# Performance work log

Hardware: AMD Instinct MI355X
Metric: run time of the kernel (lower is better)

Reference implementation:

```python
import jax, jax.numpy as jnp
import numpy as np

B, TE, TD, EH, DH = 128, 512, 128, 512, 512
K_CNN, C_CNN = 7, 105

def setup_inputs() -> dict:
    key = jax.random.key(0)
    ks = jax.random.split(key, 20)
    n = lambda k, shp: jax.random.normal(k, shp, dtype=jnp.float32) * 0.05
    return {
        "LSTM": jax.random.normal(ks[0], (B, TE, EH), dtype=jnp.float32),
        "CNNs": jax.random.normal(ks[1], (B, K_CNN, C_CNN), dtype=jnp.float32),
        "Wa_w": n(ks[2], (TD, DH)), "Wa_b": n(ks[3], (TD,)),
        "Ua_w": n(ks[4], (TE, EH)), "Ua_b": n(ks[5], (TE,)),
        "va_w": n(ks[6], (1, TE + TD)), "va_b": n(ks[7], (1,)),
        "phi_w": n(ks[8], (EH, TE)), "phi_b": n(ks[9], (EH,)),
        "Wih": n(ks[10], (4 * DH, C_CNN + EH)), "Whh": n(ks[11], (4 * DH, DH)),
        "bih": n(ks[12], (4 * DH,)), "bhh": n(ks[13], (4 * DH,)),
        "wij_w": n(ks[14], (K_CNN, DH + C_CNN)), "wij_b": n(ks[15], (K_CNN,)),
        "s_i": jax.random.uniform(ks[16], (B, DH), dtype=jnp.float32),
        "m_i": jax.random.uniform(ks[17], (B, DH), dtype=jnp.float32),
    }

def reference(LSTM, CNNs, Wa_w, Wa_b, Ua_w, Ua_b, va_w, va_b, phi_w, phi_b,
              Wih, Whh, bih, bhh, wij_w, wij_b, s_i, m_i):
    Bn, Te, Eh = LSTM.shape
    Td = Wa_w.shape[0]
    Dh = s_i.shape[1]
    # delta_i_j for all j: strict lower-triangular one-hots [Te, Te]
    Dm = jnp.tril(jnp.ones((Te, Te), LSTM.dtype), k=-1)
    phi = Dm @ phi_w.T + phi_b                     # [Te, Eh]
    ph = phi[None, :, :] * LSTM                    # [B, Te, Eh] phi_delta * LSTM[:, j]
    Ua = jnp.einsum('bte,se->bts', ph, Ua_w) + Ua_b  # [B, Te, Te]
    Wa = s_i @ Wa_w.T + Wa_b                       # [B, Td] (same for all i, j)
    cat = jnp.concatenate([jnp.broadcast_to(Wa[:, None, :], (Bn, Te, Td)), Ua], axis=-1)
    Cw = jnp.tanh(cat) * va_w[0]                   # [B, Te, Td+Te]
    # one-hot mask picks index i + Te - j; v_a reduces to a single gathered term + bias
    idx = jnp.arange(Td)[:, None] + Te - jnp.arange(Te)[None, :]   # [Td, Te]
    e = Cw[:, jnp.arange(Te)[None, :], idx] + va_b[0]              # [B, Td, Te]
    a = jax.nn.softmax(e, axis=-1)
    c_i = jnp.einsum('bit,bte->bie', a, LSTM)      # [B, Td, Eh]
    # CNN attention (same for all decoder steps; note non-standard normalizer kept faithfully)
    w_cnn, w_s = wij_w[:, :C_CNN], wij_w[:, C_CNN:]
    ep = jnp.tanh(jnp.einsum('bkc,kc->bk', CNNs, w_cnn) + s_i @ w_s.T + wij_b)  # [B, K]
    ap = jnp.exp(ep) / jnp.sum(ep)
    c_p = jnp.einsum('bk,bkc->bc', ap, CNNs)       # [B, C_CNN]
    # LSTMCell with fixed (s_i, m_i) state => all decoder steps vectorize over i
    x = jnp.concatenate([c_i, jnp.broadcast_to(c_p[:, None, :], (Bn, Td, C_CNN))], axis=-1)
    gates = jnp.einsum('bid,gd->big', x, Wih) + bih + (s_i @ Whh.T + bhh)[:, None, :]
    ig, fg, gg, og = jnp.split(gates, 4, axis=-1)
    cnew = jax.nn.sigmoid(fg) * m_i[:, None, :] + jax.nn.sigmoid(ig) * jnp.tanh(gg)
    h = jax.nn.sigmoid(og) * jnp.tanh(cnew)        # [B, Td, Dh]
    return h
```

## Files before the change

kernel.cpp:

```cpp
#include <hip/hip_runtime.h>
#include <hip/hip_bf16.h>

#define B_   128
#define TE_  512
#define TD_  128
#define EH_  512
#define DH_  512
#define KC_  7
#define CC_  105
#define G_   2048
#define KX_  617
#define KP_  640
#define GNT  10

typedef __attribute__((ext_vector_type(8))) short bf16x8;
typedef __attribute__((ext_vector_type(4))) float f32x4;

__device__ __forceinline__ float sigm(float x){ return 1.f/(1.f + __expf(-x)); }
__device__ __forceinline__ float tanhf_fast(float x){
  float e = __expf(2.f*x);
  return 1.f - 2.f/(e + 1.f);
}

__device__ __forceinline__ unsigned short f2bf(float f){
  unsigned int u = __float_as_uint(f);
  unsigned int r = (u + 0x7fffu + ((u >> 16) & 1u)) >> 16;
  return (unsigned short)r;
}

typedef __attribute__((address_space(3))) unsigned int lds_u32_t;
typedef __attribute__((address_space(1))) const unsigned int glb_u32_t;
__device__ __forceinline__ void gload16(const void* g, void* l) {
  __builtin_amdgcn_global_load_lds((glb_u32_t*)g, (lds_u32_t*)l, 16, 0, 0);
}

static const size_t OFF_PHI  = 0;
static const size_t OFF_WA   = OFF_PHI  + (size_t)TE_*EH_*4;
static const size_t OFF_HPRE = OFF_WA   + (size_t)B_*TD_*4;
static const size_t OFF_EP   = OFF_HPRE + (size_t)B_*G_*4;
static const size_t OFF_CP   = OFF_EP   + 4096;
static const size_t OFF_ET   = ((OFF_CP + (size_t)B_*CC_*4 + 255)/256)*256;
static const size_t OFF_STAT = OFF_ET + (size_t)B_*TE_*TD_*4;
static const size_t OFF_P    = ((OFF_STAT + (size_t)2*B_*TD_*4 + 255)/256)*256;
static const size_t OFF_LT   = OFF_P  + (size_t)B_*TD_*TE_*2;
static const size_t OFF_WR   = OFF_LT + (size_t)B_*TE_*EH_*2;
static const size_t OFF_PT   = OFF_P;
static const size_t OFF_SUM  = OFF_PT + (size_t)TE_*EH_*4;
static const size_t OFF_WT   = OFF_P + (size_t)2*1024*1024;
static const size_t OFF_WAT  = OFF_P + (size_t)6*1024*1024;

__global__ __launch_bounds__(256) void k_tr(const float* __restrict__ src,
                                            float* __restrict__ dst, int R, int C) {
  int r0 = blockIdx.x * 64, c0 = blockIdx.y * 64;
  __shared__ float tile[64][65];
  int tid = threadIdx.x;
  int r = tid >> 2, c16 = (tid & 3) * 16;
  const float4* s4 = (const float4*)(src + (size_t)(r0 + r)*C + c0 + c16);
  float4 v0 = s4[0], v1 = s4[1], v2 = s4[2], v3 = s4[3];
  *(float4*)&tile[r][c16]    = v0;
  *(float4*)&tile[r][c16+4]  = v1;
  *(float4*)&tile[r][c16+8]  = v2;
  *(float4*)&tile[r][c16+12] = v3;
  __syncthreads();
  float o[16];
  #pragma unroll
  for (int j = 0; j < 16; ++j) o[j] = tile[c16+j][r];
  float* d = dst + (size_t)(c0 + r)*R + r0 + c16;
  *(float4*)d      = *(float4*)&o[0];
  *(float4*)(d+4)  = *(float4*)&o[4];
  *(float4*)(d+8)  = *(float4*)&o[8];
  *(float4*)(d+12) = *(float4*)&o[12];
}

__global__ void k_phiA(const float* __restrict__ phiT, float* __restrict__ phi,
                       float* __restrict__ sums) {
  int e = blockIdx.x * 256 + threadIdx.x;
  int z = blockIdx.y;
  float acc = 0.f;
  for (int t = z*64; t < z*64 + 64; ++t) {
    phi[(size_t)t*EH_ + e] = acc;
    acc += phiT[(size_t)t*EH_ + e];
  }
  sums[z*EH_ + e] = acc;
}
__global__ void k_phiB(const float* __restrict__ sums, const float* __restrict__ phi_b,
                       float* __restrict__ phi) {
  int e = blockIdx.x * 256 + threadIdx.x;
  int z = blockIdx.y;
  float off = phi_b[e];
  for (int zz = 0; zz < z; ++zz) off += sums[zz*EH_ + e];
  for (int t = z*64; t < z*64 + 64; ++t)
    phi[(size_t)t*EH_ + e] += off;
}

__global__ __launch_bounds__(256) void k_wa2(const float* __restrict__ s_i,
                                             const float* __restrict__ WaT,
                                             const float* __restrict__ Wa_b,
                                             const float* __restrict__ va_w,
                                             float* __restrict__ wa) {
  int lane = threadIdx.x & 63, wv = threadIdx.x >> 6;
  int b = blockIdx.x * 4 + wv;
  int d0 = lane * 2;
  const float2* w = (const float2*)WaT + lane;
  const float* s = s_i + (size_t)b*DH_;
  float ax = 0.f, ay = 0.f;
  #pragma unroll 8
  for (int k = 0; k < DH_; ++k) {
    float2 wv2 = w[(size_t)k*64];
    float x = s[k];
    ax += wv2.x * x; ay += wv2.y * x;
  }
  wa[b*TD_ + d0]     = tanhf_fast(ax + Wa_b[d0])     * va_w[d0];
  wa[b*TD_ + d0 + 1] = tanhf_fast(ay + Wa_b[d0 + 1]) * va_w[d0 + 1];
}

__global__ __launch_bounds__(256) void k_hpre2(const float* __restrict__ s_i,
                                               const float* __restrict__ WhhT,
                                               const float* __restrict__ bih,
                                               const float* __restrict__ bhh,
                                               float* __restrict__ hpre) {
  int gq = blockIdx.x * 256 + threadIdx.x;
  int b  = blockIdx.y;
  const float4* w = (const float4*)WhhT + gq;
  const float* s = s_i + (size_t)b*DH_;
  float4 a = {0.f,0.f,0.f,0.f};
  #pragma unroll 8
  for (int k = 0; k < DH_; ++k) {
    float4 wv = w[(size_t)k*512];
    float x = s[k];
    a.x += wv.x*x; a.y += wv.y*x; a.z += wv.z*x; a.w += wv.w*x;
  }
  int g = gq * 4;
  float4 bi = *(const float4*)(bih + g);
  float4 bh = *(const float4*)(bhh + g);
  float4 o;
  o.x = a.x + bi.x + bh.x; o.y = a.y + bi.y + bh.y;
  o.z = a.z + bi.z + bh.z; o.w = a.w + bi.w + bh.w;
  *(float4*)(hpre + (size_t)b*G_ + g) = o;
}

__global__ __launch_bounds__(256) void k_ep(const float* __restrict__ CNNs,
                                            const float* __restrict__ wij_w,
                                            const float* __restrict__ wij_b,
                                            const float* __restrict__ s_i,
                                            float* __restrict__ ep) {
  int gw = blockIdx.x * 4 + (threadIdx.x >> 6);
  int lane = threadIdx.x & 63;
  if (gw >= B_*KC_) return;
  int b = gw / KC_, k = gw % KC_;
  const float* cr = CNNs + (size_t)(b*KC_ + k)*CC_;
  const float* wr = wij_w + (size_t)k*KX_;
  float acc = 0.f;
  for (int c = lane; c < CC_; c += 64) acc += cr[c] * wr[c];
  const float* sr = s_i + (size_t)b*DH_;
  const float* wsr = wr + CC_;
  #pragma unroll
  for (int j = 0; j < 8; ++j) { int h = lane + j*64; acc += sr[h] * wsr[h]; }
  #pragma unroll
  for (int m = 32; m; m >>= 1) acc += __shfl_xor(acc, m, 64);
  if (lane == 0) ep[gw] = tanhf_fast(acc + wij_b[k]);
}

__global__ void k_epsum(const float* __restrict__ ep, float* __restrict__ epsum) {
  __shared__ float red[1024];
  int tid = threadIdx.x;
  red[tid] = (tid < B_*KC_) ? ep[tid] : 0.f;
  __syncthreads();
  for (int off = 512; off > 0; off >>= 1) {
    if (tid < off) red[tid] += red[tid + off];
    __syncthreads();
  }
  if (tid == 0) epsum[0] = red[0];
}

__global__ __launch_bounds__(128) void k_cp(const float* __restrict__ ep,
                                            const float* __restrict__ epsum,
                                            const float* __restrict__ CNNs,
                                            unsigned short* __restrict__ X) {
  int b = blockIdx.x, c = threadIdx.x;
  float S = epsum[0];
  float apl[KC_];
  #pragma unroll
  for (int k = 0; k < KC_; ++k) apl[k] = __expf(ep[b*KC_ + k]) / S;
  float acc = 0.f;
  if (c < CC_) {
    #pragma unroll
    for (int k = 0; k < KC_; ++k)
      acc += apl[k] * CNNs[(size_t)(b*KC_ + k)*CC_ + c];
  }
  unsigned short o = (c < CC_) ? f2bf(acc) : 0;
  unsigned short* xb = X + (size_t)b*TD_*KP_ + EH_ + c;
  for (int i = 0; i < TD_; ++i)
    xb[(size_t)i*KP_] = o;
}

__global__ void k_cvtW(const float* __restrict__ Wih, unsigned short* __restrict__ Wr) {
  int id = blockIdx.x * 256 + threadIdx.x;
  int nr = id / 80, c8 = (id % 80) * 8;
  int gate = nr & 3, dh = nr >> 2;
  const float* src = Wih + (size_t)(gate*DH_ + dh)*KX_;
  unsigned short o[8];
  #pragma unroll
  for (int j = 0; j < 8; ++j) {
    int col = c8 + j;
    o[j] = (col < KX_) ? f2bf(src[col]) : 0;
  }
  *(uint4*)(Wr + (size_t)nr*KP_ + c8) = *(uint4*)o;
}

__global__ __launch_bounds__(256) void k_ltrans(const float* __restrict__ LSTM,
                                                unsigned short* __restrict__ LT) {
  int e0 = blockIdx.x * 64, t0 = blockIdx.y * 64, b = blockIdx.z;
  __shared__ float tile[64][65];
  int tid = threadIdx.x;
  int tt = tid >> 2, c16 = (tid & 3) * 16;
  const float4* src = (const float4*)(LSTM + ((size_t)b*TE_ + t0 + tt)*EH_ + e0 + c16);
  float4 v0 = src[0], v1 = src[1], v2 = src[2], v3 = src[3];
  *(float4*)&tile[tt][c16]    = v0;
  *(float4*)&tile[tt][c16+4]  = v1;
  *(float4*)&tile[tt][c16+8]  = v2;
  *(float4*)&tile[tt][c16+12] = v3;
  __syncthreads();
  int e = tid >> 2, t16 = (tid & 3) * 16;
  unsigned short o[16];
  #pragma unroll
  for (int j = 0; j < 16; ++j) o[j] = f2bf(tile[t16+j][e]);
  unsigned short* dst = LT + ((size_t)b*EH_ + e0 + e)*TE_ + t0 + t16;
  *(uint4*)dst     = *(uint4*)&o[0];
  *(uint4*)(dst+8) = *(uint4*)&o[8];
}

#define BMM_M 64
#define LDA_  40
#define LDB_  40
#define OTS_  132
__global__ __launch_bounds__(256) void k_bandmm(const float* __restrict__ LSTM,
                                                const float* __restrict__ phi,
                                                const float* __restrict__ Ua_w,
                                                const float* __restrict__ Ua_b,
                                                const float* __restrict__ va_w,
                                                const float* __restrict__ va_b,
                                                const float* __restrict__ wa,
                                                float* __restrict__ ET) {
  int t0 = blockIdx.x * BMM_M;
  int b  = blockIdx.y;
  int s_base = 321 - t0;
  __shared__ __align__(16) char smem[BMM_M * OTS_ * 4];
  short* sA = (short*)smem;
  short* sB = (short*)(smem + BMM_M*LDA_*2);
  int tid = threadIdx.x;
  int wave = tid >> 6, lane = tid & 63;
  int quad = lane >> 4, l16 = lane & 15;

  f32x4 acc[4][3];
  #pragma unroll
  for (int m = 0; m < 4; ++m)
    #pragma unroll
    for (int n = 0; n < 3; ++n)
      acc[m][n] = (f32x4){0.f, 0.f, 0.f, 0.f};

  int arow = tid >> 2;
  int ach  = (tid & 3) * 8;
  int aq   = ach >> 2;

  const float4* baseL = (const float4*)(LSTM + ((size_t)b*TE_ + t0 + arow)*EH_);
  const float4* baseP = (const float4*)(phi + (size_t)(t0 + arow)*EH_);
  const float4* baseU[3];
  int brow[3], bch[3];
  #pragma unroll
  for (int c = 0; c < 3; ++c) {
    int idx = c*256 + tid;
    brow[c] = idx >> 2;
    bch[c]  = (idx & 3) * 8;
    int s = s_base + brow[c];
    int sc = s < 0 ? 0 : (s > 511 ? 511 : s);
    baseU[c] = (const float4*)(Ua_w + (size_t)sc*EH_ + bch[c]);
  }

  float4 l0 = baseL[aq], l1 = baseL[aq+1], p0 = baseP[aq], p1 = baseP[aq+1];
  float4 u0[3], u1[3];
  #pragma unroll
  for (int c = 0; c < 3; ++c) { u0[c] = baseU[c][0]; u1[c] = baseU[c][1]; }

  for (int k0 = 0; k0 < EH_; k0 += 32) {
    unsigned short at[8];
    at[0]=f2bf(l0.x*p0.x); at[1]=f2bf(l0.y*p0.y); at[2]=f2bf(l0.z*p0.z); at[3]=f2bf(l0.w*p0.w);
    at[4]=f2bf(l1.x*p1.x); at[5]=f2bf(l1.y*p1.y); at[6]=f2bf(l1.z*p1.z); at[7]=f2bf(l1.w*p1.w);
    unsigned short bt[3][8];
    #pragma unroll
    for (int c = 0; c < 3; ++c) {
      bt[c][0]=f2bf(u0[c].x); bt[c][1]=f2bf(u0[c].y); bt[c][2]=f2bf(u0[c].z); bt[c][3]=f2bf(u0[c].w);
      bt[c][4]=f2bf(u1[c].x); bt[c][5]=f2bf(u1[c].y); bt[c][6]=f2bf(u1[c].z); bt[c][7]=f2bf(u1[c].w);
    }
    if (k0 + 32 < EH_) {
      int q = (k0 + 32) >> 2;
      l0 = baseL[q+aq]; l1 = baseL[q+aq+1]; p0 = baseP[q+aq]; p1 = baseP[q+aq+1];
      #pragma unroll
      for (int c = 0; c < 3; ++c) { u0[c] = baseU[c][q]; u1[c] = baseU[c][q+1]; }
    }
    __syncthreads();
    *(uint4*)&sA[arow*LDA_ + ach] = *(uint4*)at;
    #pragma unroll
    for (int c = 0; c < 3; ++c)
      *(uint4*)&sB[brow[c]*LDB_ + bch[c]] = *(uint4*)bt[c];
    __syncthreads();
    bf16x8 bfr[3];
    #pragma unroll
    for (int n = 0; n < 3; ++n)
      bfr[n] = *(const bf16x8*)&sB[(l16 + (wave*3 + n)*16)*LDB_ + quad*8];
    #pragma unroll
    for (int m = 0; m < 4; ++m) {
      bf16x8 af = *(const bf16x8*)&sA[(l16 + m*16)*LDA_ + quad*8];
      #pragma unroll
      for (int n = 0; n < 3; ++n)
        acc[m][n] = __builtin_amdgcn_mfma_f32_16x16x32_bf16(af, bfr[n], acc[m][n], 0, 0, 0);
    }
  }

  __syncthreads();
  float* tileO = (float*)smem;
  float vb = va_b[0];
  #pragma unroll
  for (int n = 0; n < 3; ++n) {
    int s = s_base + wave*48 + n*16 + l16;
    float ub = (s >= 0 && s < TE_) ? Ua_b[s] : 0.f;
    float vw = (s >= 0 && s < TE_) ? va_w[TD_ + s] : 0.f;
    #pragma unroll
    for (int m = 0; m < 4; ++m) {
      #pragma unroll
      for (int r = 0; r < 4; ++r) {
        int tl = m*16 + quad*4 + r;
        int i = s + t0 + tl - 384;
        if (i >= 0 && i < TD_) {
          float val;
          if (s >= 0) val = tanhf_fast(acc[m][n][r] + ub) * vw + vb;
          else        val = wa[b*TD_ + s + 128] + vb;
          tileO[tl*OTS_ + i] = val;
        }
      }
    }
  }
  __syncthreads();
  {
    int rsub = tid >> 5, c4 = (tid & 31) * 4;
    #pragma unroll
    for (int p = 0; p < 8; ++p) {
      int row = p*8 + rsub;
      float4 v = *(const float4*)&tileO[row*OTS_ + c4];
      *(float4*)(ET + ((size_t)b*TE_ + t0 + row)*TD_ + c4) = v;
    }
  }
}

#define SMX_LD 65
__global__ __launch_bounds__(512) void k_smx(const float* __restrict__ ET,
                                             unsigned short* __restrict__ P) {
  int i0 = blockIdx.x * 64, b = blockIdx.y;
  __shared__ float tile[TE_][SMX_LD];
  __shared__ float red[8][64], smax[64], sinv[64];
  int tid = threadIdx.x;

  {
    int r = tid >> 2, c16 = (tid & 3) * 16;
    #pragma unroll
    for (int rep = 0; rep < 4; ++rep) {
      int t = rep*128 + r;
      const float4* s4 = (const float4*)(ET + ((size_t)b*TE_ + t)*TD_ + i0 + c16);
      float4 v0 = s4[0], v1 = s4[1], v2 = s4[2], v3 = s4[3];
      *(float4*)&tile[t][c16]    = v0;
      *(float4*)&tile[t][c16+4]  = v1;
      *(float4*)&tile[t][c16+8]  = v2;
      *(float4*)&tile[t][c16+12] = v3;
    }
  }
  __syncthreads();

  int i = tid & 63, seg = tid >> 6;
  {
    float m = -1e30f;
    for (int t = seg*64; t < seg*64 + 64; ++t) m = fmaxf(m, tile[t][i]);
    red[seg][i] = m;
  }
  __syncthreads();
  if (tid < 64) {
    float m = red[0][tid];
    #pragma unroll
    for (int s = 1; s < 8; ++s) m = fmaxf(m, red[s][tid]);
    smax[tid] = m;
  }
  __syncthreads();
  {
    float mm = smax[i];
    float s = 0.f;
    for (int t = seg*64; t < seg*64 + 64; ++t) {
      float v = __expf(tile[t][i] - mm);
      tile[t][i] = v;
      s += v;
    }
    red[seg][i] = s;
  }
  __syncthreads();
  if (tid < 64) {
    float s = red[0][tid];
    #pragma unroll
    for (int sg = 1; sg < 8; ++sg) s += red[sg][tid];
    sinv[tid] = 1.f / s;
  }
  __syncthreads();
  {
    int tidq = tid & 255, half = tid >> 8;
    int ii = tidq >> 2, t16 = (tidq & 3) * 16;
    float inv = sinv[ii];
    #pragma unroll
    for (int tt = 0; tt < 4; ++tt) {
      int tb = (tt*2 + half) * 64;
      unsigned short o[16];
      #pragma unroll
      for (int j = 0; j < 16; ++j)
        o[j] = f2bf(tile[tb + t16 + j][ii] * inv);
      unsigned short* dst = P + ((size_t)b*TD_ + i0 + ii)*TE_ + tb + t16;
      *(uint4*)dst     = *(uint4*)&o[0];
      *(uint4*)(dst+8) = *(uint4*)&o[8];
    }
  }
}

#define CI_LD 40
__global__ __launch_bounds__(256) void k_ci_mm(const unsigned short* __restrict__ P,
                                               const unsigned short* __restrict__ LT,
                                               unsigned short* __restrict__ X) {
  int b = blockIdx.x, e0 = blockIdx.y * 128;
  __shared__ short sA[128 * CI_LD];
  __shared__ short sB[128 * CI_LD];
  int tid = threadIdx.x;
  int wave = tid >> 6, lane = tid & 63, quad = lane >> 4, l16 = lane & 15;
  int wm = wave >> 1, wn = wave & 1;
  int row = tid >> 1, ho = (tid & 1) * 16;

  const unsigned short* pa = P + ((size_t)b*TD_ + row)*TE_ + ho;
  const unsigned short* pb = LT + ((size_t)b*EH_ + e0 + row)*TE_ + ho;

  f32x4 acc[4][4];
  #pragma unroll
  for (int m = 0; m < 4; ++m)
    #pragma unroll
    for (int n = 0; n < 4; ++n)
      acc[m][n] = (f32x4){0.f, 0.f, 0.f, 0.f};

  uint4 a0 = *(const uint4*)pa, a1 = *(const uint4*)(pa + 8);
  uint4 b0 = *(const uint4*)pb, b1 = *(const uint4*)(pb + 8);

  for (int k0 = 0; k0 < TE_; k0 += 32) {
    uint4 na0, na1, nb0, nb1;
    if (k0 + 32 < TE_) {
      na0 = *(const uint4*)(pa + k0 + 32); na1 = *(const uint4*)(pa + k0 + 40);
      nb0 = *(const uint4*)(pb + k0 + 32); nb1 = *(const uint4*)(pb + k0 + 40);
    }
    __syncthreads();
    *(uint4*)&sA[row*CI_LD + ho]     = a0;
    *(uint4*)&sA[row*CI_LD + ho + 8] = a1;
    *(uint4*)&sB[row*CI_LD + ho]     = b0;
    *(uint4*)&sB[row*CI_LD + ho + 8] = b1;
    __syncthreads();
    bf16x8 bfr[4];
    #pragma unroll
    for (int n = 0; n < 4; ++n)
      bfr[n] = *(const bf16x8*)&sB[(wn*64 + n*16 + l16)*CI_LD + quad*8];
    #pragma unroll
    for (int m = 0; m < 4; ++m) {
      bf16x8 af = *(const bf16x8*)&sA[(wm*64 + m*16 + l16)*CI_LD + quad*8];
      #pragma unroll
      for (int n = 0; n < 4; ++n)
        acc[m][n] = __builtin_amdgcn_mfma_f32_16x16x32_bf16(af, bfr[n], acc[m][n], 0, 0, 0);
    }
    a0 = na0; a1 = na1; b0 = nb0; b1 = nb1;
  }

  #pragma unroll
  for (int m = 0; m < 4; ++m) {
    int i = wm*64 + m*16 + quad*4;
    #pragma unroll
    for (int n = 0; n < 4; ++n) {
      int e = e0 + wn*64 + n*16 + l16;
      unsigned short* xp = X + ((size_t)b*TD_ + i)*KP_ + e;
      #pragma unroll
      for (int r = 0; r < 4; ++r)
        xp[(size_t)r*KP_] = f2bf(acc[m][n][r]);
    }
  }
}

__global__ __launch_bounds__(512, 2) void k_gates8(const unsigned short* __restrict__ Wr,
                                                   const unsigned short* __restrict__ X,
                                                   const float* __restrict__ hpre,
                                                   const float* __restrict__ m_i,
                                                   float* __restrict__ out) {
  __shared__ short lds[4 * 256 * 64];
  const int g0  = blockIdx.x * 256;
  const int mi0 = blockIdx.y * 256;
  const int tid  = threadIdx.x;
  const int wave = tid >> 6, lane = tid & 63;
  const int l16 = lane & 15, quad = lane >> 4;
  const int wr = wave >> 2, wc = wave & 3;

  const int srow8 = lane >> 3;
  const int sch   = (lane & 7) ^ srow8;
  const unsigned short* gA = Wr + (size_t)(g0  + wave*8 + srow8) * KP_ + sch*8;
  const unsigned short* gB = X  + (size_t)(mi0 + wave*8 + srow8) * KP_ + sch*8;
  short* lA0 = lds;
  short* lB0 = lds + 16384;
  short* lA1 = lds + 32768;
  short* lB1 = lds + 49152;

  f32x4 acc[8][4];
  #pragma unroll
  for (int m = 0; m < 8; ++m)
    #pragma unroll
    for (int n = 0; n < 4; ++n) acc[m][n] = (f32x4){0.f, 0.f, 0.f, 0.f};

  auto stage = [&](int kt, int bf) {
    short* la = bf ? lA1 : lA0;
    short* lb = bf ? lB1 : lB0;
    const unsigned short* ga = gA + kt*64;
    const unsigned short* gb = gB + kt*64;
    #pragma unroll
    for (int r = 0; r < 4; ++r) {
      gload16(ga + (size_t)r*64*KP_, la + (r*8 + wave)*512);
      gload16(gb + (size_t)r*64*KP_, lb + (r*8 + wave)*512);
    }
  };

  stage(0, 0);
  __syncthreads();

  const int x7 = l16 & 7;
  for (int kt = 0; kt < GNT; ++kt) {
    const int cur = kt & 1;
    if (kt + 1 < GNT) stage(kt + 1, cur ^ 1);
    const short* la = cur ? lA1 : lA0;
    const short* lb = cur ? lB1 : lB0;
    #pragma unroll
    for (int ks = 0; ks < 2; ++ks) {
      const int ck = ((((ks << 2) | quad) ^ x7) << 3);
      bf16x8 bv[4];
      #pragma unroll
      for (int n = 0; n < 4; ++n)
        bv[n] = *(const bf16x8*)&lb[(wc*64 + n*16 + l16)*64 + ck];
      #pragma unroll
      for (int qm = 0; qm < 2; ++qm) {
        bf16x8 av[4];
        #pragma unroll
        for (int m = 0; m < 4; ++m)
          av[m] = *(const bf16x8*)&la[(wr*128 + qm*64 + m*16 + l16)*64 + ck];
        __builtin_amdgcn_s_setprio(1);
        #pragma unroll
        for (int m = 0; m < 4; ++m)
          #pragma unroll
          for (int n = 0; n < 4; ++n)
            acc[qm*4 + m][n] = __builtin_amdgcn_mfma_f32_16x16x32_bf16(av[m], bv[n], acc[qm*4 + m][n], 0, 0, 0);
        __builtin_amdgcn_s_setprio(0);
      }
    }
    __syncthreads();
  }

  const int bb = (mi0 >> 7) + (wc >> 1);
  const float* hp = hpre + (size_t)bb * G_;
  #pragma unroll
  for (int M = 0; M < 8; ++M) {
    const int dh = (g0 >> 2) + wr*32 + M*4 + quad;
    float h0 = hp[dh], h1 = hp[DH_ + dh], h2 = hp[2*DH_ + dh], h3 = hp[3*DH_ + dh];
    float miv = m_i[(size_t)bb*DH_ + dh];
    #pragma unroll
    for (int n = 0; n < 4; ++n) {
      int mi = mi0 + wc*64 + n*16 + l16;
      float ig = acc[M][n][0] + h0;
      float fg = acc[M][n][1] + h1;
      float gg = acc[M][n][2] + h2;
      float og = acc[M][n][3] + h3;
      float c  = sigm(fg)*miv + sigm(ig)*tanhf_fast(gg);
      float h  = sigm(og)*tanhf_fast(c);
      out[(size_t)mi*DH_ + dh] = h;
    }
  }
}

extern "C" void kernel_launch(void* const* d_in, const int* in_sizes, int n_in,
                              void* d_out, int out_size, void* d_ws, size_t ws_size,
                              hipStream_t stream) {
  (void)in_sizes; (void)n_in; (void)out_size; (void)ws_size;
  const float* LSTM  = (const float*)d_in[0];
  const float* CNNs  = (const float*)d_in[1];
  const float* Wa_w  = (const float*)d_in[2];
  const float* Wa_b  = (const float*)d_in[3];
  const float* Ua_w  = (const float*)d_in[4];
  const float* Ua_b  = (const float*)d_in[5];
  const float* va_w  = (const float*)d_in[6];
  const float* va_b  = (const float*)d_in[7];
  const float* phi_w = (const float*)d_in[8];
  const float* phi_b = (const float*)d_in[9];
  const float* Wih   = (const float*)d_in[10];
  const float* Whh   = (const float*)d_in[11];
  const float* bih   = (const float*)d_in[12];
  const float* bhh   = (const float*)d_in[13];
  const float* wij_w = (const float*)d_in[14];
  const float* wij_b = (const float*)d_in[15];
  const float* s_i   = (const float*)d_in[16];
  const float* m_i   = (const float*)d_in[17];
  float* out = (float*)d_out;
  char* ws = (char*)d_ws;

  float* phi  = (float*)(ws + OFF_PHI);
  float* wa   = (float*)(ws + OFF_WA);
  float* hpre = (float*)(ws + OFF_HPRE);
  float* ep   = (float*)(ws + OFF_EP);
  float* epsum= (float*)(ws + OFF_EP) + 1000;
  float* ET   = (float*)(ws + OFF_ET);
  unsigned short* X  = (unsigned short*)(ws + OFF_ET);
  unsigned short* P  = (unsigned short*)(ws + OFF_P);
  unsigned short* LT = (unsigned short*)(ws + OFF_LT);
  unsigned short* Wr = (unsigned short*)(ws + OFF_WR);
  float* phiT        = (float*)(ws + OFF_PT);
  float* sums        = (float*)(ws + OFF_SUM);
  float* WhhT        = (float*)(ws + OFF_WT);
  float* WaT         = (float*)(ws + OFF_WAT);

  k_tr      <<<dim3(8,8),      dim3(256),  0, stream>>>(phi_w, phiT, 512, 512);
  k_tr      <<<dim3(32,8),     dim3(256),  0, stream>>>(Whh, WhhT, 2048, 512);
  k_tr      <<<dim3(2,8),      dim3(256),  0, stream>>>(Wa_w, WaT, 128, 512);
  k_phiA    <<<dim3(2,8),      dim3(256),  0, stream>>>(phiT, phi, sums);
  k_phiB    <<<dim3(2,8),      dim3(256),  0, stream>>>(sums, phi_b, phi);
  k_wa2     <<<dim3(32),       dim3(256),  0, stream>>>(s_i, WaT, Wa_b, va_w, wa);
  k_hpre2   <<<dim3(2,128),    dim3(256),  0, stream>>>(s_i, WhhT, bih, bhh, hpre);
  k_ep      <<<dim3(224),      dim3(256),  0, stream>>>(CNNs, wij_w, wij_b, s_i, ep);
  k_epsum   <<<dim3(1),        dim3(1024), 0, stream>>>(ep, epsum);
  k_cvtW    <<<dim3(640),      dim3(256),  0, stream>>>(Wih, Wr);
  k_ltrans  <<<dim3(8,8,128),  dim3(256),  0, stream>>>(LSTM, LT);
  k_bandmm  <<<dim3(8,128),    dim3(256),  0, stream>>>(LSTM, phi, Ua_w, Ua_b, va_w, va_b, wa, ET);
  k_smx     <<<dim3(2,128),    dim3(512),  0, stream>>>(ET, P);
  k_cp      <<<dim3(128),      dim3(128),  0, stream>>>(ep, epsum, CNNs, X);
  k_ci_mm   <<<dim3(128,4),    dim3(256),  0, stream>>>(P, LT, X);
  k_gates8  <<<dim3(8,64),     dim3(512),  0, stream>>>(Wr, X, hpre, m_i, out);
}
```

Baseline: 489.0 us.

## Fuse softmax exp into band matmul epilogue and defer normalization to ci matmul

The band matmul epilogue now applies exp directly, writes unnormalized bf16 probabilities P, and emits per-tile partial row sums. This removes the separate softmax kernel and the fp32 ET round trip through global memory. A tiny kernel reduces the partial sums to reciprocals, which the c_i matmul applies to its output rows. No max subtraction is done, which is safe only because the logits are bounded (tanh times small weights plus bias). The unnormalized values are rounded to bf16 before scaling, which slightly changes numerics.

```diff
diff --git a/kernel.cpp b/kernel.cpp
--- a/kernel.cpp
+++ b/kernel.cpp
@@ -44,6 +44,7 @@
 static const size_t OFF_P    = ((OFF_STAT + (size_t)2*B_*TD_*4 + 255)/256)*256;
 static const size_t OFF_LT   = OFF_P  + (size_t)B_*TD_*TE_*2;
 static const size_t OFF_WR   = OFF_LT + (size_t)B_*TE_*EH_*2;
+static const size_t OFF_SP   = OFF_WR + (size_t)G_*KP_*2;
 static const size_t OFF_PT   = OFF_P;
 static const size_t OFF_SUM  = OFF_PT + (size_t)TE_*EH_*4;
 static const size_t OFF_WT   = OFF_P + (size_t)2*1024*1024;
@@ -241,7 +242,8 @@
                                                 const float* __restrict__ va_w,
                                                 const float* __restrict__ va_b,
                                                 const float* __restrict__ wa,
-                                                float* __restrict__ ET) {
+                                                unsigned short* __restrict__ P,
+                                                float* __restrict__ sums_p) {
   int t0 = blockIdx.x * BMM_M;
   int b  = blockIdx.y;
   int s_base = 321 - t0;
@@ -335,99 +337,45 @@
           float val;
           if (s >= 0) val = tanhf_fast(acc[m][n][r] + ub) * vw + vb;
           else        val = wa[b*TD_ + s + 128] + vb;
-          tileO[tl*OTS_ + i] = val;
+          tileO[tl*OTS_ + i] = __expf(val);
         }
       }
     }
   }
   __syncthreads();
+  if (tid < TD_) {
+    float ssum = 0.f;
+    #pragma unroll 8
+    for (int tl = 0; tl < 64; ++tl) ssum += tileO[tl*OTS_ + tid];
+    sums_p[((size_t)b*8 + blockIdx.x)*TD_ + tid] = ssum;
+  }
   {
-    int rsub = tid >> 5, c4 = (tid & 31) * 4;
-    #pragma unroll
-    for (int p = 0; p < 8; ++p) {
-      int row = p*8 + rsub;
-      float4 v = *(const float4*)&tileO[row*OTS_ + c4];
-      *(float4*)(ET + ((size_t)b*TE_ + t0 + row)*TD_ + c4) = v;
-    }
-  }
-}
-
-#define SMX_LD 65
-__global__ __launch_bounds__(512) void k_smx(const float* __restrict__ ET,
-                                             unsigned short* __restrict__ P) {
-  int i0 = blockIdx.x * 64, b = blockIdx.y;
-  __shared__ float tile[TE_][SMX_LD];
-  __shared__ float red[8][64], smax[64], sinv[64];
-  int tid = threadIdx.x;
-
-  {
-    int r = tid >> 2, c16 = (tid & 3) * 16;
-    #pragma unroll
-    for (int rep = 0; rep < 4; ++rep) {
-      int t = rep*128 + r;
-      const float4* s4 = (const float4*)(ET + ((size_t)b*TE_ + t)*TD_ + i0 + c16);
-      float4 v0 = s4[0], v1 = s4[1], v2 = s4[2], v3 = s4[3];
-      *(float4*)&tile[t][c16]    = v0;
-      *(float4*)&tile[t][c16+4]  = v1;
-      *(float4*)&tile[t][c16+8]  = v2;
-      *(float4*)&tile[t][c16+12] = v3;
-    }
-  }
-  __syncthreads();
-
-  int i = tid & 63, seg = tid >> 6;
-  {
-    float m = -1e30f;
-    for (int t = seg*64; t < seg*64 + 64; ++t) m = fmaxf(m, tile[t][i]);
-    red[seg][i] = m;
-  }
-  __syncthreads();
-  if (tid < 64) {
-    float m = red[0][tid];
-    #pragma unroll
-    for (int s = 1; s < 8; ++s) m = fmaxf(m, red[s][tid]);
-    smax[tid] = m;
-  }
-  __syncthreads();
-  {
-    float mm = smax[i];
-    float s = 0.f;
-    for (int t = seg*64; t < seg*64 + 64; ++t) {
-      float v = __expf(tile[t][i] - mm);
-      tile[t][i] = v;
-      s += v;
-    }
-    red[seg][i] = s;
-  }
-  __syncthreads();
-  if (tid < 64) {
-    float s = red[0][tid];
-    #pragma unroll
-    for (int sg = 1; sg < 8; ++sg) s += red[sg][tid];
-    sinv[tid] = 1.f / s;
-  }
-  __syncthreads();
-  {
-    int tidq = tid & 255, half = tid >> 8;
-    int ii = tidq >> 2, t16 = (tidq & 3) * 16;
-    float inv = sinv[ii];
-    #pragma unroll
-    for (int tt = 0; tt < 4; ++tt) {
-      int tb = (tt*2 + half) * 64;
-      unsigned short o[16];
-      #pragma unroll
-      for (int j = 0; j < 16; ++j)
-        o[j] = f2bf(tile[tb + t16 + j][ii] * inv);
-      unsigned short* dst = P + ((size_t)b*TD_ + i0 + ii)*TE_ + tb + t16;
-      *(uint4*)dst     = *(uint4*)&o[0];
-      *(uint4*)(dst+8) = *(uint4*)&o[8];
-    }
-  }
+    int ii = tid >> 1, hf = tid & 1;
+    unsigned short o[32];
+    #pragma unroll
+    for (int j = 0; j < 32; ++j)
+      o[j] = f2bf(tileO[(hf*32 + j)*OTS_ + ii]);
+    unsigned short* dst = P + ((size_t)b*TD_ + ii)*TE_ + t0 + hf*32;
+    *(uint4*)dst      = *(uint4*)&o[0];
+    *(uint4*)(dst+8)  = *(uint4*)&o[8];
+    *(uint4*)(dst+16) = *(uint4*)&o[16];
+    *(uint4*)(dst+24) = *(uint4*)&o[24];
+  }
+}
+
+__global__ __launch_bounds__(128) void k_sinv(const float* __restrict__ sums_p,
+                                              float* __restrict__ sinv) {
+  int b = blockIdx.x, i = threadIdx.x;
+  float s = 0.f;
+  #pragma unroll
+  for (int z = 0; z < 8; ++z) s += sums_p[((size_t)b*8 + z)*TD_ + i];
+  sinv[b*TD_ + i] = 1.f / s;
 }
 
 #define CI_LD 40
 __global__ __launch_bounds__(256) void k_ci_mm(const unsigned short* __restrict__ P,
                                                const unsigned short* __restrict__ LT,
+                                               const float* __restrict__ sinv,
                                                unsigned short* __restrict__ X) {
   int b = blockIdx.x, e0 = blockIdx.y * 128;
   __shared__ short sA[128 * CI_LD];
@@ -476,16 +424,19 @@
     a0 = na0; a1 = na1; b0 = nb0; b1 = nb1;
   }
 
+  const float* sv = sinv + b*TD_;
   #pragma unroll
   for (int m = 0; m < 4; ++m) {
     int i = wm*64 + m*16 + quad*4;
+    float i0 = sv[i], i1 = sv[i+1], i2 = sv[i+2], i3 = sv[i+3];
     #pragma unroll
     for (int n = 0; n < 4; ++n) {
       int e = e0 + wn*64 + n*16 + l16;
       unsigned short* xp = X + ((size_t)b*TD_ + i)*KP_ + e;
-      #pragma unroll
-      for (int r = 0; r < 4; ++r)
-        xp[(size_t)r*KP_] = f2bf(acc[m][n][r]);
+      xp[0]              = f2bf(acc[m][n][0] * i0);
+      xp[(size_t)KP_]    = f2bf(acc[m][n][1] * i1);
+      xp[(size_t)2*KP_]  = f2bf(acc[m][n][2] * i2);
+      xp[(size_t)3*KP_]  = f2bf(acc[m][n][3] * i3);
     }
   }
 }
@@ -615,11 +566,12 @@
   float* hpre = (float*)(ws + OFF_HPRE);
   float* ep   = (float*)(ws + OFF_EP);
   float* epsum= (float*)(ws + OFF_EP) + 1000;
-  float* ET   = (float*)(ws + OFF_ET);
   unsigned short* X  = (unsigned short*)(ws + OFF_ET);
+  float* sinv        = (float*)(ws + OFF_STAT);
   unsigned short* P  = (unsigned short*)(ws + OFF_P);
   unsigned short* LT = (unsigned short*)(ws + OFF_LT);
   unsigned short* Wr = (unsigned short*)(ws + OFF_WR);
+  float* sums_p      = (float*)(ws + OFF_SP);
   float* phiT        = (float*)(ws + OFF_PT);
   float* sums        = (float*)(ws + OFF_SUM);
   float* WhhT        = (float*)(ws + OFF_WT);
@@ -636,9 +588,9 @@
   k_epsum   <<<dim3(1),        dim3(1024), 0, stream>>>(ep, epsum);
   k_cvtW    <<<dim3(640),      dim3(256),  0, stream>>>(Wih, Wr);
   k_ltrans  <<<dim3(8,8,128),  dim3(256),  0, stream>>>(LSTM, LT);
-  k_bandmm  <<<dim3(8,128),    dim3(256),  0, stream>>>(LSTM, phi, Ua_w, Ua_b, va_w, va_b, wa, ET);
-  k_smx     <<<dim3(2,128),    dim3(512),  0, stream>>>(ET, P);
+  k_bandmm  <<<dim3(8,128),    dim3(256),  0, stream>>>(LSTM, phi, Ua_w, Ua_b, va_w, va_b, wa, P, sums_p);
+  k_sinv    <<<dim3(128),      dim3(128),  0, stream>>>(sums_p, sinv);
   k_cp      <<<dim3(128),      dim3(128),  0, stream>>>(ep, epsum, CNNs, X);
-  k_ci_mm   <<<dim3(128,4),    dim3(256),  0, stream>>>(P, LT, X);
+  k_ci_mm   <<<dim3(128,4),    dim3(256),  0, stream>>>(P, LT, sinv, X);
   k_gates8  <<<dim3(8,64),     dim3(512),  0, stream>>>(Wr, X, hpre, m_i, out);
 }
```

Measured after the change: 485.5 us. No clear change (-0.7%).
